# Kernel optimization log

Hardware: AMD Instinct MI355X
Metric: run time of the kernel (lower is better)

## Reference

```python
import jax, jax.numpy as jnp
import numpy as np

B, CIN, H, W = 16, 1, 256, 256
WIDTH = 64
MODES = 32
LAYERS = 4
COUT = 1


def conv1x1(x, w, b):
    # x: [B,Ci,H,W], w: [Co,Ci], b: [Co]
    return jnp.einsum('bixy,oi->boxy', x, w) + b[None, :, None, None]


def mlp(x, w1, b1, w2, b2):
    # Conv2d(ci,mid,1) -> GELU(exact) -> Conv2d(mid,co,1)
    return conv1x1(jax.nn.gelu(conv1x1(x, w1, b1), approximate=False), w2, b2)


def spectral_conv2d(x, w1r, w1i, w2r, w2i):
    # x: [B,C,H,W]; weights: [Ci,Co,m1,m2] (real/imag parts of cfloat params)
    b, c, h, w = x.shape
    m1, m2 = w1r.shape[2], w1r.shape[3]
    co = w1r.shape[1]
    x_ft = jnp.fft.rfft2(x)  # [B,C,H,W//2+1] complex64
    w1 = w1r + 1j * w1i
    w2 = w2r + 1j * w2i
    top = jnp.einsum('bixy,ioxy->boxy', x_ft[:, :, :m1, :m2], w1)
    bot = jnp.einsum('bixy,ioxy->boxy', x_ft[:, :, -m1:, :m2], w2)
    out_ft = jnp.zeros((b, co, h, w // 2 + 1), dtype=x_ft.dtype)
    out_ft = out_ft.at[:, :, :m1, :m2].set(top).at[:, :, -m1:, :m2].set(bot)
    return jnp.fft.irfft2(out_ft, s=(h, w))


def setup_inputs() -> dict:
    key = jax.random.key(0)
    ks = iter(jax.random.split(key, 32))
    scale = 1.0 / (WIDTH * WIDTH)
    f32 = jnp.float32
    inp = {}
    inp['x'] = jax.random.normal(next(ks), (B, CIN, H, W), dtype=f32)
    # lifting 1x1 conv
    inp['p_w'] = jax.random.normal(next(ks), (WIDTH, CIN), dtype=f32) / np.sqrt(CIN)
    inp['p_b'] = jnp.zeros((WIDTH,), dtype=f32)
    # per-layer spectral weights (real/imag of uniform cfloat init)
    shp = (LAYERS, WIDTH, WIDTH, MODES, MODES)
    inp['sw1r'] = scale * jax.random.uniform(next(ks), shp, dtype=f32)
    inp['sw1i'] = scale * jax.random.uniform(next(ks), shp, dtype=f32)
    inp['sw2r'] = scale * jax.random.uniform(next(ks), shp, dtype=f32)
    inp['sw2i'] = scale * jax.random.uniform(next(ks), shp, dtype=f32)
    # per-layer channel MLP (mid_channels = WIDTH)
    inp['m1w'] = jax.random.normal(next(ks), (LAYERS, WIDTH, WIDTH), dtype=f32) / np.sqrt(WIDTH)
    inp['m1b'] = jnp.zeros((LAYERS, WIDTH), dtype=f32)
    inp['m2w'] = jax.random.normal(next(ks), (LAYERS, WIDTH, WIDTH), dtype=f32) / np.sqrt(WIDTH)
    inp['m2b'] = jnp.zeros((LAYERS, WIDTH), dtype=f32)
    # per-layer skip 1x1 conv
    inp['skw'] = jax.random.normal(next(ks), (LAYERS, WIDTH, WIDTH), dtype=f32) / np.sqrt(WIDTH)
    inp['skb'] = jnp.zeros((LAYERS, WIDTH), dtype=f32)
    # projection MLP (mid = 4*WIDTH)
    inp['q1w'] = jax.random.normal(next(ks), (4 * WIDTH, WIDTH), dtype=f32) / np.sqrt(WIDTH)
    inp['q1b'] = jnp.zeros((4 * WIDTH,), dtype=f32)
    inp['q2w'] = jax.random.normal(next(ks), (COUT, 4 * WIDTH), dtype=f32) / np.sqrt(4 * WIDTH)
    inp['q2b'] = jnp.zeros((COUT,), dtype=f32)
    return inp


def reference(x, p_w, p_b, sw1r, sw1i, sw2r, sw2i, m1w, m1b, m2w, m2b,
              skw, skb, q1w, q1b, q2w, q2b):
    h = conv1x1(x, p_w, p_b)  # lift to [B,WIDTH,H,W]
    for l in range(LAYERS):
        x1 = spectral_conv2d(h, sw1r[l], sw1i[l], sw2r[l], sw2i[l])
        x1 = mlp(x1, m1w[l], m1b[l], m2w[l], m2b[l])
        x2 = conv1x1(h, skw[l], skb[l])
        h = x1 + x2
        if l < LAYERS - 1:
            h = jax.nn.gelu(h, approximate=False)
    return mlp(h, q1w, q1b, q2w, q2b)  # [B,COUT,H,W]
```

## Files before the change

kernel.cpp:

```cpp
#include <hip/hip_runtime.h>
#include <math.h>

#define NC 64
#define NH 256
#define NW 256
#define NM 32
#define NKY 64
#define HW 65536

typedef short bfrag __attribute__((ext_vector_type(8)));
typedef float facc  __attribute__((ext_vector_type(4)));
#define MFMA(a,b,c) __builtin_amdgcn_mfma_f32_16x16x32_bf16(a,b,c,0,0,0)

static constexpr float PI_F = 3.14159265358979323846f;

__device__ __forceinline__ unsigned short f2b(float f) {
  unsigned b = __float_as_uint(f);
  return (unsigned short)((b + 0x7FFFu + ((b >> 16) & 1u)) >> 16);
}
__device__ __forceinline__ float b2f(unsigned short h) {
  return __uint_as_float((unsigned)h << 16);
}

__device__ __forceinline__ float gelu_f(float x) {
  float z = fabsf(x) * 0.70710678118654752f;
  float t = 1.0f / (1.0f + 0.3275911f * z);
  float e = __expf(-z * z);
  float p = t * (0.254829592f + t * (-0.284496736f + t * (1.421413741f +
            t * (-1.453152027f + t * 1.061405429f))));
  float er = copysignf(1.0f - p * e, x);
  return 0.5f * x * (1.0f + er);
}

__global__ void k_tEy(unsigned short* __restrict__ eh, unsigned short* __restrict__ el) {
  int i = blockIdx.x * 256 + threadIdx.x;
  int m = i >> 8, y = i & 255;
  int kyi = m & 63;
  int ky = (kyi < 32) ? kyi : (192 + kyi);
  int a = (ky * y) & 255;
  float s, c; sincosf((float)a * (PI_F / 128.f), &s, &c);
  float v = (m < 64) ? c : -s;
  unsigned short h = f2b(v);
  eh[i] = h; el[i] = f2b(v - b2f(h));
}
__global__ void k_tEx(unsigned short* __restrict__ eh, unsigned short* __restrict__ el) {
  int i = blockIdx.x * 256 + threadIdx.x;
  int m = i >> 9, k = i & 511;
  int x = k & 255, plane = k >> 8, kx = m & 31;
  int a = (kx * x) & 255;
  float s, c; sincosf((float)a * (PI_F / 128.f), &s, &c);
  float v = (m < 32) ? (plane ? s : c) : (plane ? c : -s);
  unsigned short h = f2b(v);
  eh[i] = h; el[i] = f2b(v - b2f(h));
}
__global__ void k_tWy(unsigned short* __restrict__ eh, unsigned short* __restrict__ el) {
  int i = blockIdx.x * 256 + threadIdx.x;
  int row = i >> 7, k = i & 127;
  int y = row & 255, part = row >> 8;
  int kyi = k & 63, plane = k >> 6;
  int ky = (kyi < 32) ? kyi : (192 + kyi);
  int a = (ky * y) & 255;
  float s, c; sincosf((float)a * (PI_F / 128.f), &s, &c);
  float v = (part == 0) ? (plane ? -s : c) : (plane ? c : s);
  unsigned short h = f2b(v);
  eh[i] = h; el[i] = f2b(v - b2f(h));
}
__global__ void k_tCx(unsigned short* __restrict__ eh, unsigned short* __restrict__ el) {
  int i = blockIdx.x * 256 + threadIdx.x;
  int x = i >> 6, k = i & 63;
  int kx = k & 31, plane = k >> 5;
  float w = ((kx == 0) ? 1.0f : 2.0f) / 65536.0f;
  int a = (kx * x) & 255;
  float s, c; sincosf((float)a * (PI_F / 128.f), &s, &c);
  float v = plane ? (-w * s) : (w * c);
  unsigned short h = f2b(v);
  eh[i] = h; el[i] = f2b(v - b2f(h));
}

__global__ void k_cvt2(const float* __restrict__ src, unsigned short* __restrict__ hi,
                       unsigned short* __restrict__ lo, int n) {
  int i = blockIdx.x * 256 + threadIdx.x;
  if (i < n) {
    float v = src[i];
    unsigned short h = f2b(v);
    hi[i] = h;
    lo[i] = f2b(v - b2f(h));
  }
}

__global__ __launch_bounds__(256) void k_lift(const float* __restrict__ x,
                                              const float* __restrict__ pw,
                                              const float* __restrict__ pb,
                                              unsigned short* __restrict__ hh,
                                              unsigned short* __restrict__ hl) {
  int b = blockIdx.y;
  int yx = blockIdx.x * 256 + threadIdx.x;
  float v = x[(size_t)b * HW + yx];
  size_t o = (size_t)b * NC * HW + yx;
  for (int c = 0; c < NC; ++c) {
    float u = v * pw[c] + pb[c];
    unsigned short hi = f2b(u);
    hh[o + (size_t)c * HW] = hi;
    hl[o + (size_t)c * HW] = f2b(u - b2f(hi));
  }
}

__global__ __launch_bounds__(256) void k_fy2(const unsigned short* __restrict__ hh,
                                             const unsigned short* __restrict__ hl,
                                             const unsigned short* __restrict__ Ah,
                                             const unsigned short* __restrict__ Al,
                                             float* __restrict__ Xc, int Ncol) {
  int tid = threadIdx.x, wv = tid >> 6, ln = tid & 63, g16 = ln >> 4, l15 = ln & 15;
  int colbase = blockIdx.x * 128 + wv * 32;
  facc acc[8][2];
#pragma unroll
  for (int mf = 0; mf < 8; ++mf)
#pragma unroll
    for (int pf = 0; pf < 2; ++pf) acc[mf][pf] = (facc)0.f;
#pragma unroll 1
  for (int ks = 0; ks < 8; ++ks) {
    int kof = g16 * 8 + 32 * ks;
    bfrag bh[2], bl[2];
#pragma unroll
    for (int pf = 0; pf < 2; ++pf) {
      int col = colbase + pf * 16 + l15;
      size_t o = (size_t)(col >> 8) * HW + (col & 255) + (size_t)kof * 256;
#pragma unroll
      for (int j = 0; j < 8; ++j) {
        bh[pf][j] = (short)hh[o + j * 256];
        bl[pf][j] = (short)hl[o + j * 256];
      }
    }
#pragma unroll
    for (int mf = 0; mf < 8; ++mf) {
      int row = 16 * mf + l15;
      bfrag ah = *(const bfrag*)(Ah + row * 256 + kof);
      bfrag al = *(const bfrag*)(Al + row * 256 + kof);
#pragma unroll
      for (int pf = 0; pf < 2; ++pf) {
        acc[mf][pf] = MFMA(ah, bh[pf], acc[mf][pf]);
        acc[mf][pf] = MFMA(ah, bl[pf], acc[mf][pf]);
        acc[mf][pf] = MFMA(al, bh[pf], acc[mf][pf]);
      }
    }
  }
#pragma unroll
  for (int mf = 0; mf < 8; ++mf)
#pragma unroll
    for (int pf = 0; pf < 2; ++pf) {
      int col = colbase + pf * 16 + l15;
#pragma unroll
      for (int r = 0; r < 4; ++r)
        Xc[(size_t)(16 * mf + 4 * g16 + r) * Ncol + col] = acc[mf][pf][r];
    }
}

__global__ __launch_bounds__(256) void k_fx2(const float* __restrict__ Xc,
                                             const unsigned short* __restrict__ Ah,
                                             const unsigned short* __restrict__ Al,
                                             float* __restrict__ X2r,
                                             float* __restrict__ X2i, int NcXc) {
  int tid = threadIdx.x, wv = tid >> 6, ln = tid & 63, g16 = ln >> 4, l15 = ln & 15;
  int colbase = blockIdx.x * 64 + wv * 16;
  facc acc[4];
#pragma unroll
  for (int mf = 0; mf < 4; ++mf) acc[mf] = (facc)0.f;
#pragma unroll 1
  for (int ks = 0; ks < 16; ++ks) {
    int plane = ks >> 3;
    int x0 = (ks & 7) * 32 + g16 * 8;
    int kof = g16 * 8 + 32 * ks;
    bfrag bh, bl;
    {
      int col = colbase + l15;
      const float* p = Xc + (size_t)(plane * 64 + (col & 63)) * NcXc + (col >> 6) * 256 + x0;
      float4 u0 = *(const float4*)p;
      float4 u1 = *(const float4*)(p + 4);
      float tv[8] = {u0.x, u0.y, u0.z, u0.w, u1.x, u1.y, u1.z, u1.w};
#pragma unroll
      for (int j = 0; j < 8; ++j) {
        unsigned short hi = f2b(tv[j]);
        bh[j] = (short)hi;
        bl[j] = (short)f2b(tv[j] - b2f(hi));
      }
    }
#pragma unroll
    for (int mf = 0; mf < 4; ++mf) {
      int row = 16 * mf + l15;
      bfrag ah = *(const bfrag*)(Ah + row * 512 + kof);
      bfrag al = *(const bfrag*)(Al + row * 512 + kof);
      acc[mf] = MFMA(ah, bh, acc[mf]);
      acc[mf] = MFMA(ah, bl, acc[mf]);
      acc[mf] = MFMA(al, bh, acc[mf]);
    }
  }
#pragma unroll
  for (int mf = 0; mf < 4; ++mf) {
    int col = colbase + l15;
    float* base = (mf >= 2) ? X2i : X2r;
    int kxb = 16 * (mf & 1) + 4 * g16;
    float4 v = make_float4(acc[mf][0], acc[mf][1], acc[mf][2], acc[mf][3]);
    *(float4*)(base + (size_t)col * 32 + kxb) = v;
  }
}

__global__ __launch_bounds__(512) void k_spec(const float* __restrict__ X2r,
                                              const float* __restrict__ X2i,
                                              const float* __restrict__ w1r,
                                              const float* __restrict__ w1i,
                                              const float* __restrict__ w2r,
                                              const float* __restrict__ w2i,
                                              float* __restrict__ S, int Ncs) {
  int b = blockIdx.y;
  int och = blockIdx.x & 3;
  int kyi = blockIdx.x >> 2;
  __shared__ float2 xs[NC * NM];
  for (int idx = threadIdx.x; idx < NC * NM; idx += 512) {
    int i = idx >> 5, kx = idx & 31;
    size_t c2 = ((size_t)(b * 64 + i) * 64 + kyi) * 32 + kx;
    xs[idx] = make_float2(X2r[c2], X2i[c2]);
  }
  __syncthreads();
  int kx = threadIdx.x & 31;
  int ol = threadIdx.x >> 5;
  int o = och * 16 + ol;
  int kym = kyi & 31;
  const float* wr = (kyi < 32) ? w1r : w2r;
  const float* wi = (kyi < 32) ? w1i : w2i;
  size_t wb = ((size_t)o * NM + kym) * NM + kx;
  float ar = 0.f, ai = 0.f;
#pragma unroll 4
  for (int i = 0; i < NC; ++i) {
    float2 xv = xs[i * NM + kx];
    float wrv = wr[wb + (size_t)i * 65536];
    float wiv = wi[wb + (size_t)i * 65536];
    ar += xv.x * wrv - xv.y * wiv;
    ai += xv.x * wiv + xv.y * wrv;
  }
  size_t cco = (size_t)(b * 64 + o) * 32 + kx;
  S[(size_t)kyi * Ncs + cco] = ar;
  S[(size_t)(64 + kyi) * Ncs + cco] = ai;
}

__global__ __launch_bounds__(256) void k_iy2(const float* __restrict__ S,
                                             const unsigned short* __restrict__ Ah,
                                             const unsigned short* __restrict__ Al,
                                             float* __restrict__ t2, int Ncs) {
  int tid = threadIdx.x, wv = tid >> 6, ln = tid & 63, g16 = ln >> 4, l15 = ln & 15;
  int colbase = blockIdx.x * 128 + wv * 32;
  int rowb = blockIdx.y * 64;
  facc acc[4][2];
#pragma unroll
  for (int mf = 0; mf < 4; ++mf)
#pragma unroll
    for (int pf = 0; pf < 2; ++pf) acc[mf][pf] = (facc)0.f;
#pragma unroll 1
  for (int ks = 0; ks < 4; ++ks) {
    int kof = g16 * 8 + 32 * ks;
    bfrag bh[2], bl[2];
#pragma unroll
    for (int pf = 0; pf < 2; ++pf) {
      int col = colbase + pf * 16 + l15;
      const float* p = S + (size_t)kof * Ncs + col;
#pragma unroll
      for (int j = 0; j < 8; ++j) {
        float v = p[(size_t)j * Ncs];
        unsigned short hi = f2b(v);
        bh[pf][j] = (short)hi;
        bl[pf][j] = (short)f2b(v - b2f(hi));
      }
    }
#pragma unroll
    for (int mf = 0; mf < 4; ++mf) {
      int row = rowb + 16 * mf + l15;
      bfrag ah = *(const bfrag*)(Ah + row * 128 + kof);
      bfrag al = *(const bfrag*)(Al + row * 128 + kof);
#pragma unroll
      for (int pf = 0; pf < 2; ++pf) {
        acc[mf][pf] = MFMA(ah, bh[pf], acc[mf][pf]);
        acc[mf][pf] = MFMA(ah, bl[pf], acc[mf][pf]);
        acc[mf][pf] = MFMA(al, bh[pf], acc[mf][pf]);
      }
    }
  }
#pragma unroll
  for (int mf = 0; mf < 4; ++mf)
#pragma unroll
    for (int pf = 0; pf < 2; ++pf) {
      int col = colbase + pf * 16 + l15;
#pragma unroll
      for (int r = 0; r < 4; ++r)
        t2[(size_t)(rowb + 16 * mf + 4 * g16 + r) * Ncs + col] = acc[mf][pf][r];
    }
}

__global__ __launch_bounds__(256) void k_ix2(const float* __restrict__ t2,
                                             const unsigned short* __restrict__ Ah,
                                             const unsigned short* __restrict__ Al,
                                             unsigned short* __restrict__ x1h,
                                             unsigned short* __restrict__ x1l, int Nct) {
  int tid = threadIdx.x, wv = tid >> 6, ln = tid & 63, g16 = ln >> 4, l15 = ln & 15;
  int colbase = blockIdx.x * 128 + wv * 32;
  int rowb = blockIdx.y * 128;
  facc acc[8][2];
#pragma unroll
  for (int mf = 0; mf < 8; ++mf)
#pragma unroll
    for (int pf = 0; pf < 2; ++pf) acc[mf][pf] = (facc)0.f;
#pragma unroll 1
  for (int ks = 0; ks < 2; ++ks) {
    int kof = g16 * 8 + 32 * ks;
    bfrag bh[2], bl[2];
#pragma unroll
    for (int pf = 0; pf < 2; ++pf) {
      int col = colbase + pf * 16 + l15;
      const float* p = t2 + (size_t)(ks * 256 + (col & 255)) * Nct + (col >> 8) * 32 + g16 * 8;
      float4 u0 = *(const float4*)p;
      float4 u1 = *(const float4*)(p + 4);
      float tv[8] = {u0.x, u0.y, u0.z, u0.w, u1.x, u1.y, u1.z, u1.w};
#pragma unroll
      for (int j = 0; j < 8; ++j) {
        unsigned short hi = f2b(tv[j]);
        bh[pf][j] = (short)hi;
        bl[pf][j] = (short)f2b(tv[j] - b2f(hi));
      }
    }
#pragma unroll
    for (int mf = 0; mf < 8; ++mf) {
      int row = rowb + 16 * mf + l15;
      bfrag ah = *(const bfrag*)(Ah + row * 64 + kof);
      bfrag al = *(const bfrag*)(Al + row * 64 + kof);
#pragma unroll
      for (int pf = 0; pf < 2; ++pf) {
        acc[mf][pf] = MFMA(ah, bh[pf], acc[mf][pf]);
        acc[mf][pf] = MFMA(ah, bl[pf], acc[mf][pf]);
        acc[mf][pf] = MFMA(al, bh[pf], acc[mf][pf]);
      }
    }
  }
#pragma unroll
  for (int mf = 0; mf < 8; ++mf)
#pragma unroll
    for (int pf = 0; pf < 2; ++pf) {
      int col = colbase + pf * 16 + l15;
      int bc = col >> 8, y = col & 255;
      int xb = rowb + 16 * mf + 4 * g16;
      ushort4 hv, lv;
#pragma unroll
      for (int r = 0; r < 4; ++r) {
        float v = acc[mf][pf][r];
        unsigned short hi = f2b(v);
        ((unsigned short*)&hv)[r] = hi;
        ((unsigned short*)&lv)[r] = f2b(v - b2f(hi));
      }
      size_t o = (size_t)bc * HW + y * 256 + xb;
      *(ushort4*)(x1h + o) = hv;
      *(ushort4*)(x1l + o) = lv;
    }
}

__global__ __launch_bounds__(256) void k_mlp1s(unsigned short* __restrict__ x1h,
                                               unsigned short* __restrict__ x1l,
                                               const unsigned short* __restrict__ w1h,
                                               const unsigned short* __restrict__ w1l,
                                               const float* __restrict__ b1p) {
  __shared__ unsigned short whs[64 * 72], wls[64 * 72];
  int tid = threadIdx.x;
  for (int i = tid; i < 64 * 64; i += 256) {
    int r = i >> 6, c = i & 63;
    whs[r * 72 + c] = w1h[i];
    wls[r * 72 + c] = w1l[i];
  }
  int wv = tid >> 6, ln = tid & 63, g16 = ln >> 4, l15 = ln & 15;
  int b = blockIdx.y;
  unsigned short* xh = x1h + (size_t)b * NC * HW;
  unsigned short* xl = x1l + (size_t)b * NC * HW;
  float b1v[4][4];
#pragma unroll
  for (int mf = 0; mf < 4; ++mf)
#pragma unroll
    for (int r = 0; r < 4; ++r) b1v[mf][r] = b1p[16 * mf + 4 * g16 + r];
  __syncthreads();
  for (int t = 0; t < 4; ++t) {
    int pxb = (blockIdx.x * 4 + t) * 128 + wv * 32;
    facc a1[4][2];
#pragma unroll
    for (int mf = 0; mf < 4; ++mf)
#pragma unroll
      for (int pf = 0; pf < 2; ++pf) {
        facc z; z[0] = b1v[mf][0]; z[1] = b1v[mf][1]; z[2] = b1v[mf][2]; z[3] = b1v[mf][3];
        a1[mf][pf] = z;
      }
#pragma unroll
    for (int ks = 0; ks < 2; ++ks) {
      bfrag xhb[2], xlb[2];
#pragma unroll
      for (int pf = 0; pf < 2; ++pf) {
        int px = pxb + pf * 16 + l15;
#pragma unroll
        for (int j = 0; j < 8; ++j) {
          int c = g16 * 8 + j + 32 * ks;
          xhb[pf][j] = (short)xh[(size_t)c * HW + px];
          xlb[pf][j] = (short)xl[(size_t)c * HW + px];
        }
      }
#pragma unroll
      for (int mf = 0; mf < 4; ++mf) {
        bfrag wh = *(const bfrag*)(whs + (16 * mf + l15) * 72 + g16 * 8 + 32 * ks);
        bfrag wl = *(const bfrag*)(wls + (16 * mf + l15) * 72 + g16 * 8 + 32 * ks);
#pragma unroll
        for (int pf = 0; pf < 2; ++pf) {
          a1[mf][pf] = MFMA(wh, xhb[pf], a1[mf][pf]);
          a1[mf][pf] = MFMA(wh, xlb[pf], a1[mf][pf]);
          a1[mf][pf] = MFMA(wl, xhb[pf], a1[mf][pf]);
        }
      }
    }
#pragma unroll
    for (int mf = 0; mf < 4; ++mf)
#pragma unroll
      for (int pf = 0; pf < 2; ++pf) {
        int px = pxb + pf * 16 + l15;
#pragma unroll
        for (int r = 0; r < 4; ++r) {
          float v = gelu_f(a1[mf][pf][r]);
          unsigned short hi = f2b(v);
          size_t idx = (size_t)(16 * mf + 4 * g16 + r) * HW + px;
          xh[idx] = hi;
          xl[idx] = f2b(v - b2f(hi));
        }
      }
  }
}

__global__ __launch_bounds__(256) void k_mix2(const unsigned short* __restrict__ midh,
                                              const unsigned short* __restrict__ midl,
                                              unsigned short* __restrict__ hh_,
                                              unsigned short* __restrict__ hl_,
                                              const unsigned short* __restrict__ w2h,
                                              const unsigned short* __restrict__ w2l,
                                              const unsigned short* __restrict__ skh,
                                              const unsigned short* __restrict__ skl,
                                              const float* __restrict__ b2p,
                                              const float* __restrict__ skbp,
                                              int do_gelu) {
  __shared__ unsigned short w2hs[64 * 72], w2ls[64 * 72], skhs[64 * 72], skls[64 * 72];
  int tid = threadIdx.x;
  for (int i = tid; i < 64 * 64; i += 256) {
    int r = i >> 6, c = i & 63;
    w2hs[r * 72 + c] = w2h[i];
    w2ls[r * 72 + c] = w2l[i];
    skhs[r * 72 + c] = skh[i];
    skls[r * 72 + c] = skl[i];
  }
  int wv = tid >> 6, ln = tid & 63, g16 = ln >> 4, l15 = ln & 15;
  int b = blockIdx.y;
  const unsigned short* mh = midh + (size_t)b * NC * HW;
  const unsigned short* ml = midl + (size_t)b * NC * HW;
  unsigned short* hbh = hh_ + (size_t)b * NC * HW;
  unsigned short* hbl = hl_ + (size_t)b * NC * HW;
  float b2v[4][4];
#pragma unroll
  for (int mf = 0; mf < 4; ++mf)
#pragma unroll
    for (int r = 0; r < 4; ++r) {
      int o = 16 * mf + 4 * g16 + r;
      b2v[mf][r] = b2p[o] + skbp[o];
    }
  __syncthreads();
  for (int t = 0; t < 4; ++t) {
    int pxb = (blockIdx.x * 4 + t) * 128 + wv * 32;
    facc a2[4][2];
#pragma unroll
    for (int mf = 0; mf < 4; ++mf)
#pragma unroll
      for (int pf = 0; pf < 2; ++pf) {
        facc z; z[0] = b2v[mf][0]; z[1] = b2v[mf][1]; z[2] = b2v[mf][2]; z[3] = b2v[mf][3];
        a2[mf][pf] = z;
      }
#pragma unroll
    for (int ks = 0; ks < 2; ++ks) {
      bfrag mhb[2], mlb[2], hhb[2], hlb[2];
#pragma unroll
      for (int pf = 0; pf < 2; ++pf) {
        int px = pxb + pf * 16 + l15;
#pragma unroll
        for (int j = 0; j < 8; ++j) {
          int c = g16 * 8 + j + 32 * ks;
          mhb[pf][j] = (short)mh[(size_t)c * HW + px];
          mlb[pf][j] = (short)ml[(size_t)c * HW + px];
          hhb[pf][j] = (short)hbh[(size_t)c * HW + px];
          hlb[pf][j] = (short)hbl[(size_t)c * HW + px];
        }
      }
#pragma unroll
      for (int mf = 0; mf < 4; ++mf) {
        bfrag w2hf = *(const bfrag*)(w2hs + (16 * mf + l15) * 72 + g16 * 8 + 32 * ks);
        bfrag w2lf = *(const bfrag*)(w2ls + (16 * mf + l15) * 72 + g16 * 8 + 32 * ks);
        bfrag skhf = *(const bfrag*)(skhs + (16 * mf + l15) * 72 + g16 * 8 + 32 * ks);
        bfrag sklf = *(const bfrag*)(skls + (16 * mf + l15) * 72 + g16 * 8 + 32 * ks);
#pragma unroll
        for (int pf = 0; pf < 2; ++pf) {
          a2[mf][pf] = MFMA(w2hf, mhb[pf], a2[mf][pf]);
          a2[mf][pf] = MFMA(w2hf, mlb[pf], a2[mf][pf]);
          a2[mf][pf] = MFMA(w2lf, mhb[pf], a2[mf][pf]);
          a2[mf][pf] = MFMA(skhf, hhb[pf], a2[mf][pf]);
          a2[mf][pf] = MFMA(skhf, hlb[pf], a2[mf][pf]);
          a2[mf][pf] = MFMA(sklf, hhb[pf], a2[mf][pf]);
        }
      }
    }
#pragma unroll
    for (int mf = 0; mf < 4; ++mf)
#pragma unroll
      for (int pf = 0; pf < 2; ++pf) {
        facc v = a2[mf][pf];
        if (do_gelu) {
          v[0] = gelu_f(v[0]); v[1] = gelu_f(v[1]);
          v[2] = gelu_f(v[2]); v[3] = gelu_f(v[3]);
        }
        int px = pxb + pf * 16 + l15;
#pragma unroll
        for (int r = 0; r < 4; ++r) {
          float u = v[r];
          unsigned short hi = f2b(u);
          size_t idx = (size_t)(16 * mf + 4 * g16 + r) * HW + px;
          hbh[idx] = hi;
          hbl[idx] = f2b(u - b2f(hi));
        }
      }
  }
}

__global__ __launch_bounds__(256) void k_pproj(const unsigned short* __restrict__ hh,
                                               const unsigned short* __restrict__ hl,
                                               const unsigned short* __restrict__ q1h,
                                               const unsigned short* __restrict__ q1l,
                                               const float* __restrict__ q1bp,
                                               const float* __restrict__ q2wp,
                                               const float* __restrict__ q2bp,
                                               float* __restrict__ out,
                                               int R0, int accum) {
  __shared__ unsigned short q1sh[128 * 72];
  __shared__ unsigned short q1sl[128 * 72];
  __shared__ float q1bs[128], q2s[128];
  int tid = threadIdx.x;
  for (int i = tid; i < 2048; i += 256) {
    int row = i >> 4, c4 = (i & 15) * 4;
    ushort4 vh = *(const ushort4*)(q1h + (size_t)(R0 + row) * 64 + c4);
    ushort4 vl = *(const ushort4*)(q1l + (size_t)(R0 + row) * 64 + c4);
    *(ushort4*)(q1sh + row * 72 + c4) = vh;
    *(ushort4*)(q1sl + row * 72 + c4) = vl;
  }
  if (tid < 128) {
    q1bs[tid] = q1bp[R0 + tid];
    q2s[tid] = q2wp[R0 + tid];
  }
  int wv = tid >> 6, ln = tid & 63, g16 = ln >> 4, l15 = ln & 15;
  float q2bias = q2bp[0];
  __syncthreads();

  int colbase = blockIdx.x * 128 + wv * 32;
  facc acc[8][2];
#pragma unroll
  for (int mf = 0; mf < 8; ++mf)
#pragma unroll
    for (int pf = 0; pf < 2; ++pf) {
      facc z;
#pragma unroll
      for (int r = 0; r < 4; ++r) z[r] = q1bs[16 * mf + 4 * g16 + r];
      acc[mf][pf] = z;
    }
#pragma unroll
  for (int ks = 0; ks < 2; ++ks) {
    bfrag bh[2], bl[2];
#pragma unroll
    for (int pf = 0; pf < 2; ++pf) {
      int col = colbase + pf * 16 + l15;
      size_t o = (size_t)(col >> 16) * NC * HW + (col & 65535);
#pragma unroll
      for (int j = 0; j < 8; ++j) {
        int c = g16 * 8 + j + 32 * ks;
        bh[pf][j] = (short)hh[o + (size_t)c * HW];
        bl[pf][j] = (short)hl[o + (size_t)c * HW];
      }
    }
#pragma unroll
    for (int mf = 0; mf < 8; ++mf) {
      bfrag ah = *(const bfrag*)(q1sh + (16 * mf + l15) * 72 + g16 * 8 + 32 * ks);
      bfrag al = *(const bfrag*)(q1sl + (16 * mf + l15) * 72 + g16 * 8 + 32 * ks);
#pragma unroll
      for (int pf = 0; pf < 2; ++pf) {
        acc[mf][pf] = MFMA(ah, bh[pf], acc[mf][pf]);
        acc[mf][pf] = MFMA(ah, bl[pf], acc[mf][pf]);
        acc[mf][pf] = MFMA(al, bh[pf], acc[mf][pf]);
      }
    }
  }
#pragma unroll
  for (int pf = 0; pf < 2; ++pf) {
    float partial = 0.f;
#pragma unroll
    for (int mf = 0; mf < 8; ++mf)
#pragma unroll
      for (int r = 0; r < 4; ++r)
        partial += gelu_f(acc[mf][pf][r]) * q2s[16 * mf + 4 * g16 + r];
    partial += __shfl_xor(partial, 16);
    partial += __shfl_xor(partial, 32);
    if (ln < 16) {
      int col = colbase + pf * 16 + ln;
      if (accum) out[col] += partial;
      else out[col] = partial + q2bias;
    }
  }
}

extern "C" void kernel_launch(void* const* d_in, const int* in_sizes, int n_in,
                              void* d_out, int out_size, void* d_ws, size_t ws_size,
                              hipStream_t stream) {
  const float* x    = (const float*)d_in[0];
  const float* p_w  = (const float*)d_in[1];
  const float* p_b  = (const float*)d_in[2];
  const float* sw1r = (const float*)d_in[3];
  const float* sw1i = (const float*)d_in[4];
  const float* sw2r = (const float*)d_in[5];
  const float* sw2i = (const float*)d_in[6];
  const float* m1w  = (const float*)d_in[7];
  const float* m1b  = (const float*)d_in[8];
  const float* m2w  = (const float*)d_in[9];
  const float* m2b  = (const float*)d_in[10];
  const float* skw  = (const float*)d_in[11];
  const float* skb  = (const float*)d_in[12];
  const float* q1w  = (const float*)d_in[13];
  const float* q1b  = (const float*)d_in[14];
  const float* q2w  = (const float*)d_in[15];
  const float* q2b  = (const float*)d_in[16];

  const size_t MB = 1048576ULL;
  const size_t TBL = 1 * MB;
  int g = 16;
  while (g > 1 && (size_t)g * 36 * MB + TBL > ws_size) g >>= 1;
  if ((size_t)g * 36 * MB + TBL > ws_size) return;

  char* wsb = (char*)d_ws;
  unsigned short* Eyh = (unsigned short*)(wsb + 0);
  unsigned short* Eyl = (unsigned short*)(wsb + 65536);
  unsigned short* Exh = (unsigned short*)(wsb + 131072);
  unsigned short* Exl = (unsigned short*)(wsb + 196608);
  unsigned short* Wyh = (unsigned short*)(wsb + 262144);
  unsigned short* Wyl = (unsigned short*)(wsb + 393216);
  unsigned short* Cxh = (unsigned short*)(wsb + 524288);
  unsigned short* Cxl = (unsigned short*)(wsb + 557056);
  unsigned short* m1h = (unsigned short*)(wsb + 589824);
  unsigned short* m1l = (unsigned short*)(wsb + 622592);
  unsigned short* m2h = (unsigned short*)(wsb + 655360);
  unsigned short* m2l = (unsigned short*)(wsb + 688128);
  unsigned short* skh = (unsigned short*)(wsb + 720896);
  unsigned short* skl = (unsigned short*)(wsb + 753664);
  unsigned short* q1h = (unsigned short*)(wsb + 786432);
  unsigned short* q1l = (unsigned short*)(wsb + 819200);

  char* base = wsb + TBL;
  unsigned short* Hh = (unsigned short*)base;
  unsigned short* Hl = (unsigned short*)(base + (size_t)g * 8 * MB);
  unsigned short* x1h = (unsigned short*)(base + (size_t)g * 16 * MB);
  unsigned short* x1l = (unsigned short*)(base + (size_t)g * 24 * MB);
  float* Xc  = (float*)x1h;
  float* X2r = (float*)x1l;
  float* X2i = (float*)((char*)x1l + (size_t)g * 512 * 1024);
  float* S   = (float*)((char*)x1l + (size_t)g * 1 * MB);
  float* t2  = (float*)(base + (size_t)g * 32 * MB);

  k_tEy<<<128, 256, 0, stream>>>(Eyh, Eyl);
  k_tEx<<<128, 256, 0, stream>>>(Exh, Exl);
  k_tWy<<<256, 256, 0, stream>>>(Wyh, Wyl);
  k_tCx<<<64, 256, 0, stream>>>(Cxh, Cxl);
  k_cvt2<<<64, 256, 0, stream>>>(m1w, m1h, m1l, 16384);
  k_cvt2<<<64, 256, 0, stream>>>(m2w, m2h, m2l, 16384);
  k_cvt2<<<64, 256, 0, stream>>>(skw, skh, skl, 16384);
  k_cvt2<<<64, 256, 0, stream>>>(q1w, q1h, q1l, 16384);

  int Nfy = g * 16384;
  int Ncs = g * 2048;

  for (int b0 = 0; b0 < 16; b0 += g) {
    k_lift<<<dim3(256, g), 256, 0, stream>>>(x + (size_t)b0 * HW, p_w, p_b, Hh, Hl);
    for (int l = 0; l < 4; ++l) {
      k_fy2<<<g * 128, 256, 0, stream>>>(Hh, Hl, Eyh, Eyl, Xc, Nfy);
      k_fx2<<<g * 64, 256, 0, stream>>>(Xc, Exh, Exl, X2r, X2i, Nfy);
      k_spec<<<dim3(256, g), 512, 0, stream>>>(X2r, X2i,
                                               sw1r + (size_t)l * 4194304,
                                               sw1i + (size_t)l * 4194304,
                                               sw2r + (size_t)l * 4194304,
                                               sw2i + (size_t)l * 4194304, S, Ncs);
      k_iy2<<<dim3(g * 16, 8), 256, 0, stream>>>(S, Wyh, Wyl, t2, Ncs);
      k_ix2<<<dim3(g * 128, 2), 256, 0, stream>>>(t2, Cxh, Cxl, x1h, x1l, Ncs);
      k_mlp1s<<<dim3(128, g), 256, 0, stream>>>(x1h, x1l, m1h + l * 4096, m1l + l * 4096,
                                                m1b + l * 64);
      k_mix2<<<dim3(128, g), 256, 0, stream>>>(x1h, x1l, Hh, Hl, m2h + l * 4096, m2l + l * 4096,
                                               skh + l * 4096, skl + l * 4096,
                                               m2b + l * 64, skb + l * 64, (l < 3) ? 1 : 0);
    }
    float* outc = (float*)d_out + (size_t)b0 * HW;
    k_pproj<<<g * 512, 256, 0, stream>>>(Hh, Hl, q1h, q1l, q1b, q2w, q2b, outc, 0, 0);
    k_pproj<<<g * 512, 256, 0, stream>>>(Hh, Hl, q1h, q1l, q1b, q2w, q2b, outc, 128, 1);
  }
}
```

Measured before the change: 4.245 ms.

## Fuse channel MLP and skip mix into one kernel, pack hidden hi/lo pairs

```diff
diff --git a/kernel.cpp b/kernel.cpp
--- a/kernel.cpp
+++ b/kernel.cpp
@@ -20,6 +20,11 @@
 }
 __device__ __forceinline__ float b2f(unsigned short h) {
   return __uint_as_float((unsigned)h << 16);
+}
+__device__ __forceinline__ unsigned packsplit(float v) {
+  unsigned short hi = f2b(v);
+  unsigned short lo = f2b(v - b2f(hi));
+  return (unsigned)hi | ((unsigned)lo << 16);
 }
 
 __device__ __forceinline__ float gelu_f(float x) {
@@ -91,22 +96,16 @@
 __global__ __launch_bounds__(256) void k_lift(const float* __restrict__ x,
                                               const float* __restrict__ pw,
                                               const float* __restrict__ pb,
-                                              unsigned short* __restrict__ hh,
-                                              unsigned short* __restrict__ hl) {
+                                              unsigned* __restrict__ hp) {
   int b = blockIdx.y;
   int yx = blockIdx.x * 256 + threadIdx.x;
   float v = x[(size_t)b * HW + yx];
   size_t o = (size_t)b * NC * HW + yx;
-  for (int c = 0; c < NC; ++c) {
-    float u = v * pw[c] + pb[c];
-    unsigned short hi = f2b(u);
-    hh[o + (size_t)c * HW] = hi;
-    hl[o + (size_t)c * HW] = f2b(u - b2f(hi));
-  }
-}
-
-__global__ __launch_bounds__(256) void k_fy2(const unsigned short* __restrict__ hh,
-                                             const unsigned short* __restrict__ hl,
+  for (int c = 0; c < NC; ++c)
+    hp[o + (size_t)c * HW] = packsplit(v * pw[c] + pb[c]);
+}
+
+__global__ __launch_bounds__(256) void k_fy2(const unsigned* __restrict__ hp,
                                              const unsigned short* __restrict__ Ah,
                                              const unsigned short* __restrict__ Al,
                                              float* __restrict__ Xc, int Ncol) {
@@ -127,8 +126,9 @@
       size_t o = (size_t)(col >> 8) * HW + (col & 255) + (size_t)kof * 256;
 #pragma unroll
       for (int j = 0; j < 8; ++j) {
-        bh[pf][j] = (short)hh[o + j * 256];
-        bl[pf][j] = (short)hl[o + j * 256];
+        unsigned u = hp[o + j * 256];
+        bh[pf][j] = (short)(u & 0xffffu);
+        bl[pf][j] = (short)(u >> 16);
       }
     }
 #pragma unroll
@@ -359,84 +359,12 @@
     }
 }
 
-__global__ __launch_bounds__(256) void k_mlp1s(unsigned short* __restrict__ x1h,
-                                               unsigned short* __restrict__ x1l,
-                                               const unsigned short* __restrict__ w1h,
-                                               const unsigned short* __restrict__ w1l,
-                                               const float* __restrict__ b1p) {
-  __shared__ unsigned short whs[64 * 72], wls[64 * 72];
-  int tid = threadIdx.x;
-  for (int i = tid; i < 64 * 64; i += 256) {
-    int r = i >> 6, c = i & 63;
-    whs[r * 72 + c] = w1h[i];
-    wls[r * 72 + c] = w1l[i];
-  }
-  int wv = tid >> 6, ln = tid & 63, g16 = ln >> 4, l15 = ln & 15;
-  int b = blockIdx.y;
-  unsigned short* xh = x1h + (size_t)b * NC * HW;
-  unsigned short* xl = x1l + (size_t)b * NC * HW;
-  float b1v[4][4];
-#pragma unroll
-  for (int mf = 0; mf < 4; ++mf)
-#pragma unroll
-    for (int r = 0; r < 4; ++r) b1v[mf][r] = b1p[16 * mf + 4 * g16 + r];
-  __syncthreads();
-  for (int t = 0; t < 4; ++t) {
-    int pxb = (blockIdx.x * 4 + t) * 128 + wv * 32;
-    facc a1[4][2];
-#pragma unroll
-    for (int mf = 0; mf < 4; ++mf)
-#pragma unroll
-      for (int pf = 0; pf < 2; ++pf) {
-        facc z; z[0] = b1v[mf][0]; z[1] = b1v[mf][1]; z[2] = b1v[mf][2]; z[3] = b1v[mf][3];
-        a1[mf][pf] = z;
-      }
-#pragma unroll
-    for (int ks = 0; ks < 2; ++ks) {
-      bfrag xhb[2], xlb[2];
-#pragma unroll
-      for (int pf = 0; pf < 2; ++pf) {
-        int px = pxb + pf * 16 + l15;
-#pragma unroll
-        for (int j = 0; j < 8; ++j) {
-          int c = g16 * 8 + j + 32 * ks;
-          xhb[pf][j] = (short)xh[(size_t)c * HW + px];
-          xlb[pf][j] = (short)xl[(size_t)c * HW + px];
-        }
-      }
-#pragma unroll
-      for (int mf = 0; mf < 4; ++mf) {
-        bfrag wh = *(const bfrag*)(whs + (16 * mf + l15) * 72 + g16 * 8 + 32 * ks);
-        bfrag wl = *(const bfrag*)(wls + (16 * mf + l15) * 72 + g16 * 8 + 32 * ks);
-#pragma unroll
-        for (int pf = 0; pf < 2; ++pf) {
-          a1[mf][pf] = MFMA(wh, xhb[pf], a1[mf][pf]);
-          a1[mf][pf] = MFMA(wh, xlb[pf], a1[mf][pf]);
-          a1[mf][pf] = MFMA(wl, xhb[pf], a1[mf][pf]);
-        }
-      }
-    }
-#pragma unroll
-    for (int mf = 0; mf < 4; ++mf)
-#pragma unroll
-      for (int pf = 0; pf < 2; ++pf) {
-        int px = pxb + pf * 16 + l15;
-#pragma unroll
-        for (int r = 0; r < 4; ++r) {
-          float v = gelu_f(a1[mf][pf][r]);
-          unsigned short hi = f2b(v);
-          size_t idx = (size_t)(16 * mf + 4 * g16 + r) * HW + px;
-          xh[idx] = hi;
-          xl[idx] = f2b(v - b2f(hi));
-        }
-      }
-  }
-}
-
-__global__ __launch_bounds__(256) void k_mix2(const unsigned short* __restrict__ midh,
-                                              const unsigned short* __restrict__ midl,
-                                              unsigned short* __restrict__ hh_,
-                                              unsigned short* __restrict__ hl_,
+__global__ __launch_bounds__(256) void k_fmlp(const unsigned short* __restrict__ x1h,
+                                              const unsigned short* __restrict__ x1l,
+                                              unsigned* __restrict__ Hp,
+                                              const unsigned short* __restrict__ w1h,
+                                              const unsigned short* __restrict__ w1l,
+                                              const float* __restrict__ b1p,
                                               const unsigned short* __restrict__ w2h,
                                               const unsigned short* __restrict__ w2l,
                                               const unsigned short* __restrict__ skh,
@@ -444,96 +372,123 @@
                                               const float* __restrict__ b2p,
                                               const float* __restrict__ skbp,
                                               int do_gelu) {
-  __shared__ unsigned short w2hs[64 * 72], w2ls[64 * 72], skhs[64 * 72], skls[64 * 72];
-  int tid = threadIdx.x;
-  for (int i = tid; i < 64 * 64; i += 256) {
-    int r = i >> 6, c = i & 63;
-    w2hs[r * 72 + c] = w2h[i];
-    w2ls[r * 72 + c] = w2l[i];
-    skhs[r * 72 + c] = skh[i];
-    skls[r * 72 + c] = skl[i];
-  }
-  int wv = tid >> 6, ln = tid & 63, g16 = ln >> 4, l15 = ln & 15;
+  __shared__ float mids[4][64 * 33];
+  int tid = threadIdx.x, wv = tid >> 6, ln = tid & 63, g16 = ln >> 4, l15 = ln & 15;
   int b = blockIdx.y;
-  const unsigned short* mh = midh + (size_t)b * NC * HW;
-  const unsigned short* ml = midl + (size_t)b * NC * HW;
-  unsigned short* hbh = hh_ + (size_t)b * NC * HW;
-  unsigned short* hbl = hl_ + (size_t)b * NC * HW;
-  float b2v[4][4];
+  int pxb = blockIdx.x * 128 + wv * 32;
+  const unsigned short* xh = x1h + (size_t)b * NC * HW;
+  const unsigned short* xl = x1l + (size_t)b * NC * HW;
+  unsigned* hb = Hp + (size_t)b * NC * HW;
+
+  facc a1[4][2];
 #pragma unroll
   for (int mf = 0; mf < 4; ++mf)
 #pragma unroll
-    for (int r = 0; r < 4; ++r) {
-      int o = 16 * mf + 4 * g16 + r;
-      b2v[mf][r] = b2p[o] + skbp[o];
-    }
-  __syncthreads();
-  for (int t = 0; t < 4; ++t) {
-    int pxb = (blockIdx.x * 4 + t) * 128 + wv * 32;
-    facc a2[4][2];
-#pragma unroll
-    for (int mf = 0; mf < 4; ++mf)
+    for (int pf = 0; pf < 2; ++pf) {
+      facc z;
+#pragma unroll
+      for (int r = 0; r < 4; ++r) z[r] = b1p[16 * mf + 4 * g16 + r];
+      a1[mf][pf] = z;
+    }
+#pragma unroll
+  for (int ks = 0; ks < 2; ++ks) {
+    bfrag xhb[2], xlb[2];
+#pragma unroll
+    for (int pf = 0; pf < 2; ++pf) {
+      int px = pxb + pf * 16 + l15;
+#pragma unroll
+      for (int j = 0; j < 8; ++j) {
+        int c = g16 * 8 + j + 32 * ks;
+        xhb[pf][j] = (short)xh[(size_t)c * HW + px];
+        xlb[pf][j] = (short)xl[(size_t)c * HW + px];
+      }
+    }
+#pragma unroll
+    for (int mf = 0; mf < 4; ++mf) {
+      bfrag ah = *(const bfrag*)(w1h + (16 * mf + l15) * 64 + g16 * 8 + 32 * ks);
+      bfrag al = *(const bfrag*)(w1l + (16 * mf + l15) * 64 + g16 * 8 + 32 * ks);
 #pragma unroll
       for (int pf = 0; pf < 2; ++pf) {
-        facc z; z[0] = b2v[mf][0]; z[1] = b2v[mf][1]; z[2] = b2v[mf][2]; z[3] = b2v[mf][3];
-        a2[mf][pf] = z;
-      }
-#pragma unroll
-    for (int ks = 0; ks < 2; ++ks) {
-      bfrag mhb[2], mlb[2], hhb[2], hlb[2];
+        a1[mf][pf] = MFMA(ah, xhb[pf], a1[mf][pf]);
+        a1[mf][pf] = MFMA(ah, xlb[pf], a1[mf][pf]);
+        a1[mf][pf] = MFMA(al, xhb[pf], a1[mf][pf]);
+      }
+    }
+  }
+  float* mw = mids[wv];
+#pragma unroll
+  for (int mf = 0; mf < 4; ++mf)
+#pragma unroll
+    for (int pf = 0; pf < 2; ++pf)
+#pragma unroll
+      for (int r = 0; r < 4; ++r)
+        mw[(16 * mf + 4 * g16 + r) * 33 + pf * 16 + l15] = gelu_f(a1[mf][pf][r]);
+
+  facc a2[4][2];
+#pragma unroll
+  for (int mf = 0; mf < 4; ++mf)
+#pragma unroll
+    for (int pf = 0; pf < 2; ++pf) {
+      facc z;
+#pragma unroll
+      for (int r = 0; r < 4; ++r) {
+        int o = 16 * mf + 4 * g16 + r;
+        z[r] = b2p[o] + skbp[o];
+      }
+      a2[mf][pf] = z;
+    }
+#pragma unroll
+  for (int ks = 0; ks < 2; ++ks) {
+    bfrag mhb[2], mlb[2], hhb[2], hlb[2];
+#pragma unroll
+    for (int pf = 0; pf < 2; ++pf) {
+      int px = pxb + pf * 16 + l15;
+#pragma unroll
+      for (int j = 0; j < 8; ++j) {
+        int c = g16 * 8 + j + 32 * ks;
+        float v = mw[c * 33 + pf * 16 + l15];
+        unsigned short hi = f2b(v);
+        mhb[pf][j] = (short)hi;
+        mlb[pf][j] = (short)f2b(v - b2f(hi));
+        unsigned u = hb[(size_t)c * HW + px];
+        hhb[pf][j] = (short)(u & 0xffffu);
+        hlb[pf][j] = (short)(u >> 16);
+      }
+    }
+#pragma unroll
+    for (int mf = 0; mf < 4; ++mf) {
+      bfrag w2hf = *(const bfrag*)(w2h + (16 * mf + l15) * 64 + g16 * 8 + 32 * ks);
+      bfrag w2lf = *(const bfrag*)(w2l + (16 * mf + l15) * 64 + g16 * 8 + 32 * ks);
+      bfrag skhf = *(const bfrag*)(skh + (16 * mf + l15) * 64 + g16 * 8 + 32 * ks);
+      bfrag sklf = *(const bfrag*)(skl + (16 * mf + l15) * 64 + g16 * 8 + 32 * ks);
 #pragma unroll
       for (int pf = 0; pf < 2; ++pf) {
-        int px = pxb + pf * 16 + l15;
-#pragma unroll
-        for (int j = 0; j < 8; ++j) {
-          int c = g16 * 8 + j + 32 * ks;
-          mhb[pf][j] = (short)mh[(size_t)c * HW + px];
-          mlb[pf][j] = (short)ml[(size_t)c * HW + px];
-          hhb[pf][j] = (short)hbh[(size_t)c * HW + px];
-          hlb[pf][j] = (short)hbl[(size_t)c * HW + px];
-        }
-      }
-#pragma unroll
-      for (int mf = 0; mf < 4; ++mf) {
-        bfrag w2hf = *(const bfrag*)(w2hs + (16 * mf + l15) * 72 + g16 * 8 + 32 * ks);
-        bfrag w2lf = *(const bfrag*)(w2ls + (16 * mf + l15) * 72 + g16 * 8 + 32 * ks);
-        bfrag skhf = *(const bfrag*)(skhs + (16 * mf + l15) * 72 + g16 * 8 + 32 * ks);
-        bfrag sklf = *(const bfrag*)(skls + (16 * mf + l15) * 72 + g16 * 8 + 32 * ks);
-#pragma unroll
-        for (int pf = 0; pf < 2; ++pf) {
-          a2[mf][pf] = MFMA(w2hf, mhb[pf], a2[mf][pf]);
-          a2[mf][pf] = MFMA(w2hf, mlb[pf], a2[mf][pf]);
-          a2[mf][pf] = MFMA(w2lf, mhb[pf], a2[mf][pf]);
-          a2[mf][pf] = MFMA(skhf, hhb[pf], a2[mf][pf]);
-          a2[mf][pf] = MFMA(skhf, hlb[pf], a2[mf][pf]);
-          a2[mf][pf] = MFMA(sklf, hhb[pf], a2[mf][pf]);
-        }
-      }
-    }
-#pragma unroll
-    for (int mf = 0; mf < 4; ++mf)
-#pragma unroll
-      for (int pf = 0; pf < 2; ++pf) {
-        facc v = a2[mf][pf];
-        if (do_gelu) {
-          v[0] = gelu_f(v[0]); v[1] = gelu_f(v[1]);
-          v[2] = gelu_f(v[2]); v[3] = gelu_f(v[3]);
-        }
-        int px = pxb + pf * 16 + l15;
-#pragma unroll
-        for (int r = 0; r < 4; ++r) {
-          float u = v[r];
-          unsigned short hi = f2b(u);
-          size_t idx = (size_t)(16 * mf + 4 * g16 + r) * HW + px;
-          hbh[idx] = hi;
-          hbl[idx] = f2b(u - b2f(hi));
-        }
-      }
-  }
-}
-
-__global__ __launch_bounds__(256) void k_pproj(const unsigned short* __restrict__ hh,
-                                               const unsigned short* __restrict__ hl,
+        a2[mf][pf] = MFMA(w2hf, mhb[pf], a2[mf][pf]);
+        a2[mf][pf] = MFMA(w2hf, mlb[pf], a2[mf][pf]);
+        a2[mf][pf] = MFMA(w2lf, mhb[pf], a2[mf][pf]);
+        a2[mf][pf] = MFMA(skhf, hhb[pf], a2[mf][pf]);
+        a2[mf][pf] = MFMA(skhf, hlb[pf], a2[mf][pf]);
+        a2[mf][pf] = MFMA(sklf, hhb[pf], a2[mf][pf]);
+      }
+    }
+  }
+#pragma unroll
+  for (int mf = 0; mf < 4; ++mf)
+#pragma unroll
+    for (int pf = 0; pf < 2; ++pf) {
+      facc v = a2[mf][pf];
+      if (do_gelu) {
+        v[0] = gelu_f(v[0]); v[1] = gelu_f(v[1]);
+        v[2] = gelu_f(v[2]); v[3] = gelu_f(v[3]);
+      }
+      int px = pxb + pf * 16 + l15;
+#pragma unroll
+      for (int r = 0; r < 4; ++r)
+        hb[(size_t)(16 * mf + 4 * g16 + r) * HW + px] = packsplit(v[r]);
+    }
+}
+
+__global__ __launch_bounds__(256) void k_pproj(const unsigned* __restrict__ hp,
                                                const unsigned short* __restrict__ q1h,
                                                const unsigned short* __restrict__ q1l,
                                                const float* __restrict__ q1bp,
@@ -581,8 +536,9 @@
 #pragma unroll
       for (int j = 0; j < 8; ++j) {
         int c = g16 * 8 + j + 32 * ks;
-        bh[pf][j] = (short)hh[o + (size_t)c * HW];
-        bl[pf][j] = (short)hl[o + (size_t)c * HW];
+        unsigned u = hp[o + (size_t)c * HW];
+        bh[pf][j] = (short)(u & 0xffffu);
+        bl[pf][j] = (short)(u >> 16);
       }
     }
 #pragma unroll
@@ -661,8 +617,7 @@
   unsigned short* q1l = (unsigned short*)(wsb + 819200);
 
   char* base = wsb + TBL;
-  unsigned short* Hh = (unsigned short*)base;
-  unsigned short* Hl = (unsigned short*)(base + (size_t)g * 8 * MB);
+  unsigned* Hp = (unsigned*)base;
   unsigned short* x1h = (unsigned short*)(base + (size_t)g * 16 * MB);
   unsigned short* x1l = (unsigned short*)(base + (size_t)g * 24 * MB);
   float* Xc  = (float*)x1h;
@@ -684,9 +639,9 @@
   int Ncs = g * 2048;
 
   for (int b0 = 0; b0 < 16; b0 += g) {
-    k_lift<<<dim3(256, g), 256, 0, stream>>>(x + (size_t)b0 * HW, p_w, p_b, Hh, Hl);
+    k_lift<<<dim3(256, g), 256, 0, stream>>>(x + (size_t)b0 * HW, p_w, p_b, Hp);
     for (int l = 0; l < 4; ++l) {
-      k_fy2<<<g * 128, 256, 0, stream>>>(Hh, Hl, Eyh, Eyl, Xc, Nfy);
+      k_fy2<<<g * 128, 256, 0, stream>>>(Hp, Eyh, Eyl, Xc, Nfy);
       k_fx2<<<g * 64, 256, 0, stream>>>(Xc, Exh, Exl, X2r, X2i, Nfy);
       k_spec<<<dim3(256, g), 512, 0, stream>>>(X2r, X2i,
                                                sw1r + (size_t)l * 4194304,
@@ -695,14 +650,14 @@
                                                sw2i + (size_t)l * 4194304, S, Ncs);
       k_iy2<<<dim3(g * 16, 8), 256, 0, stream>>>(S, Wyh, Wyl, t2, Ncs);
       k_ix2<<<dim3(g * 128, 2), 256, 0, stream>>>(t2, Cxh, Cxl, x1h, x1l, Ncs);
-      k_mlp1s<<<dim3(128, g), 256, 0, stream>>>(x1h, x1l, m1h + l * 4096, m1l + l * 4096,
-                                                m1b + l * 64);
-      k_mix2<<<dim3(128, g), 256, 0, stream>>>(x1h, x1l, Hh, Hl, m2h + l * 4096, m2l + l * 4096,
+      k_fmlp<<<dim3(512, g), 256, 0, stream>>>(x1h, x1l, Hp,
+                                               m1h + l * 4096, m1l + l * 4096, m1b + l * 64,
+                                               m2h + l * 4096, m2l + l * 4096,
                                                skh + l * 4096, skl + l * 4096,
                                                m2b + l * 64, skb + l * 64, (l < 3) ? 1 : 0);
     }
     float* outc = (float*)d_out + (size_t)b0 * HW;
-    k_pproj<<<g * 512, 256, 0, stream>>>(Hh, Hl, q1h, q1l, q1b, q2w, q2b, outc, 0, 0);
-    k_pproj<<<g * 512, 256, 0, stream>>>(Hh, Hl, q1h, q1l, q1b, q2w, q2b, outc, 128, 1);
-  }
-}
+    k_pproj<<<g * 512, 256, 0, stream>>>(Hp, q1h, q1l, q1b, q2w, q2b, outc, 0, 0);
+    k_pproj<<<g * 512, 256, 0, stream>>>(Hp, q1h, q1l, q1b, q2w, q2b, outc, 128, 1);
+  }
+}
```

Measured after the change: 3.810 ms. 10.2% less time.
